# Performance work log

Measured on AMD Instinct MI355X. Metric: run time of the kernel, lower is better.

## Reference

```python
import jax, jax.numpy as jnp
import numpy as np

N, E, B_GRAPHS = 50000, 512000, 64
XD, ED, C, H, L = 16, 8, 64, 2, 2
EPS = 1e-5


def setup_inputs() -> dict:
    key = jax.random.key(0)
    ks = jax.random.split(key, 20)
    w = lambda k, shape: jax.random.normal(k, shape, jnp.float32) * 0.1
    return {
        "x": jax.random.normal(ks[0], (N, XD), jnp.float32),
        "edge_attr": jax.random.normal(ks[1], (E, ED), jnp.float32),
        "edge_src": jax.random.randint(ks[2], (E,), 0, N, dtype=jnp.int32),
        "edge_dst": jax.random.randint(ks[3], (E,), 0, N, dtype=jnp.int32),
        "batch": jnp.sort(jax.random.randint(ks[4], (N,), 0, B_GRAPHS, dtype=jnp.int32)),
        "node_W": w(ks[5], (XD, C)), "node_b": jnp.zeros((C,), jnp.float32),
        "edge_W": w(ks[6], (ED, C)), "edge_b": jnp.zeros((C,), jnp.float32),
        "Wq": w(ks[7], (L, C, H * C)), "bq": jnp.zeros((L, H * C), jnp.float32),
        "Wk": w(ks[8], (L, C, H * C)), "bk": jnp.zeros((L, H * C), jnp.float32),
        "Wv": w(ks[9], (L, C, H * C)), "bv": jnp.zeros((L, H * C), jnp.float32),
        "We": w(ks[10], (L, C, H * C)), "be": jnp.zeros((L, H * C), jnp.float32),
        "Wskip": w(ks[11], (L, C, C)), "bskip": jnp.zeros((L, C), jnp.float32),
        "gamma": jnp.ones((L, C), jnp.float32), "beta": jnp.zeros((L, C), jnp.float32),
        "gate_W": w(ks[12], (C, 1)), "gate_b": jnp.zeros((1,), jnp.float32),
        "out_W": w(ks[13], (C, 1)), "out_b": jnp.zeros((1,), jnp.float32),
    }


def reference(x, edge_attr, edge_src, edge_dst, batch,
              node_W, node_b, edge_W, edge_b,
              Wq, bq, Wk, bk, Wv, bv, We, be,
              Wskip, bskip, gamma, beta,
              gate_W, gate_b, out_W, out_b):
    n = x.shape[0]
    h = x @ node_W + node_b                       # node encoder: [N, C]
    e = edge_attr @ edge_W + edge_b               # edge encoder: [E, C]
    scale = 1.0 / jnp.sqrt(jnp.float32(C))
    for i in range(L):
        identity = h
        # TransformerConv (UniMP), concat=False -> mean over heads
        q = (h @ Wq[i] + bq[i]).reshape(n, H, C)
        k = (h @ Wk[i] + bk[i]).reshape(n, H, C)
        v = (h @ Wv[i] + bv[i]).reshape(n, H, C)
        ep = (e @ We[i] + be[i]).reshape(-1, H, C)
        k_e = k[edge_src] + ep                    # [E, H, C]
        v_e = v[edge_src] + ep                    # [E, H, C]
        logits = jnp.einsum('ehc,ehc->eh', q[edge_dst], k_e) * scale
        # segment softmax over incoming edges of each target node
        m = jax.ops.segment_max(logits, edge_dst, num_segments=n)
        a = jnp.exp(logits - m[edge_dst])
        denom = jax.ops.segment_sum(a, edge_dst, num_segments=n)
        alpha = a / denom[edge_dst]               # [E, H]
        agg = jax.ops.segment_sum(alpha[:, :, None] * v_e, edge_dst, num_segments=n)
        out = agg.mean(axis=1) + h @ Wskip[i] + bskip[i]   # root/skip term
        # BatchNorm1d (training mode, biased variance)
        mu = out.mean(axis=0)
        var = out.var(axis=0)
        out = gamma[i] * (out - mu) * jax.lax.rsqrt(var + EPS) + beta[i]
        out = jax.nn.leaky_relu(out, 0.01)
        h = out + identity                        # residual
    # GlobalAttention pooling over graphs
    gate = (h @ gate_W + gate_b)[:, 0]            # [N]
    gm = jax.ops.segment_max(gate, batch, num_segments=B_GRAPHS)
    ge = jnp.exp(gate - gm[batch])
    gd = jax.ops.segment_sum(ge, batch, num_segments=B_GRAPHS)
    wts = ge / gd[batch]
    pooled = jax.ops.segment_sum(wts[:, None] * h, batch, num_segments=B_GRAPHS)
    return jax.nn.sigmoid(pooled @ out_W + out_b)  # [B_GRAPHS, 1]
```

## Files before the change

### kernel.cpp

```cpp
#include <hip/hip_runtime.h>
#include <hip/hip_bf16.h>

typedef unsigned short ushort_t;
typedef __attribute__((ext_vector_type(8))) short short8;
typedef __attribute__((ext_vector_type(4))) float float4v;

__device__ __forceinline__ float bfu_lo(unsigned u) {
    return __uint_as_float(u << 16);
}
__device__ __forceinline__ float bfu_hi(unsigned u) {
    return __uint_as_float(u & 0xffff0000u);
}
__device__ __forceinline__ ushort_t f2bf(float f) {
    __hip_bfloat16 h = __float2bfloat16(f);
    return *reinterpret_cast<ushort_t*>(&h);
}



__global__ __launch_bounds__(256) void setup_kernel(
    const float* __restrict__ x, const float* __restrict__ node_W,
    const float* __restrict__ node_b,
    const float* __restrict__ edge_W, const float* __restrict__ edge_b,
    const float* __restrict__ We, const float* __restrict__ be,
    const float* __restrict__ Wq, const float* __restrict__ bq,
    const float* __restrict__ Wk, const float* __restrict__ bk,
    const float* __restrict__ Wv, const float* __restrict__ bv,
    const float* __restrict__ Wskip, const float* __restrict__ bskip,
    float* __restrict__ h, ushort_t* __restrict__ h_bf,
    int* __restrict__ counts,
    float* __restrict__ Wc, float* __restrict__ bcb,
    ushort_t* __restrict__ Wall_arr, float* __restrict__ Wall_bias,
    int O0, int O1, int O2, int N) {
    int b = blockIdx.x, t = threadIdx.x;
    if (b < O0) {
        int idx = b * 256 + t;
        if (idx < N * 64) {
            int n = idx >> 6, c = idx & 63;
            float acc = node_b[c];
#pragma unroll
            for (int j = 0; j < 16; ++j) acc += x[n * 16 + j] * node_W[j * 64 + c];
            h[idx] = acc;
            h_bf[idx] = f2bf(acc);
        }
    } else if (b < O1) {
        int i = (b - O0) * 256 + t;
        if (i < N) counts[i] = 0;
    } else if (b < O2) {
        int tid = (b - O1) * 256 + t;
        if (tid < 2048) {
            int l = tid >> 10, d = (tid >> 7) & 7, j = tid & 127;
            float s = 0.f;
            for (int m = 0; m < 64; ++m) s += edge_W[d * 64 + m] * We[l * 8192 + m * 128 + j];
            Wc[l * 1024 + d * 128 + j] = s;
        } else if (tid < 2048 + 256) {
            int u = tid - 2048;
            int l = u >> 7, j = u & 127;
            float s = be[l * 128 + j];
            for (int m = 0; m < 64; ++m) s += edge_b[m] * We[l * 8192 + m * 128 + j];
            bcb[l * 128 + j] = s;
        }
    } else {
        int tid = (b - O2) * 256 + t;
        if (tid < 2 * 28672) {
            int l = tid / 28672, u = tid % 28672;
            int j = u & 7, ln = (u >> 3) & 63, kch = (u >> 9) & 1, ct = u >> 10;
            int nn = ln & 15, quad = ln >> 4;
            int k = kch * 32 + quad * 8 + j;
            int col = ct * 16 + nn;
            float v;
            if (col < 128)      v = Wq[l * 8192 + k * 128 + col];
            else if (col < 256) v = Wk[l * 8192 + k * 128 + col - 128];
            else if (col < 384) v = Wv[l * 8192 + k * 128 + col - 256];
            else                v = Wskip[l * 4096 + k * 64 + col - 384];
            Wall_arr[(size_t)l * 32768 + ct * 1024 + kch * 512 + ln * 8 + j] = f2bf(v);
        } else if (tid < 2 * 28672 + 2 * 448) {
            int u = tid - 2 * 28672;
            int l = u / 448, col = u % 448;
            float v;
            if (col < 128)      v = bq[l * 128 + col];
            else if (col < 256) v = bk[l * 128 + col - 128];
            else if (col < 384) v = bv[l * 128 + col - 256];
            else                v = bskip[l * 64 + col - 384];
            Wall_bias[l * 512 + col] = v;
        }
    }
}

__global__ void combine2_kernel(const float* __restrict__ Wq, const float* __restrict__ bq,
                                const float* __restrict__ Wc, const float* __restrict__ bcb,
                                ushort_t* __restrict__ Wall_arr, float* __restrict__ Wall_bias) {
    int tid = blockIdx.x * 256 + threadIdx.x;
    if (tid < 2304) {
        int l = tid / 1152, u = tid % 1152, k = u / 18, j = u % 18;
        float s = 0.f;
        if (j < 16) {
            int hh = j >> 3, d = j & 7;
            for (int c = 0; c < 64; ++c)
                s += Wq[l * 8192 + k * 128 + hh * 64 + c] * Wc[l * 1024 + d * 128 + hh * 64 + c];
        } else {
            int hh = j - 16;
            for (int c = 0; c < 64; ++c)
                s += Wq[l * 8192 + k * 128 + hh * 64 + c] * bcb[l * 128 + hh * 64 + c];
        }
        s *= 0.125f;
        int col = 448 + j;
        int ct = col >> 4, nn = col & 15;
        int kch = k >> 5, quad = (k >> 3) & 3, jj = k & 7;
        int ln = quad * 16 + nn;
        Wall_arr[(size_t)l * 32768 + ct * 1024 + kch * 512 + ln * 8 + jj] = f2bf(s);
    } else if (tid < 2304 + 36) {
        int u = tid - 2304;
        int l = u / 18, j = u % 18;
        float s = 0.f;
        if (j < 16) {
            int hh = j >> 3, d = j & 7;
            for (int c = 0; c < 64; ++c)
                s += bq[l * 128 + hh * 64 + c] * Wc[l * 1024 + d * 128 + hh * 64 + c];
        } else {
            int hh = j - 16;
            for (int c = 0; c < 64; ++c)
                s += bq[l * 128 + hh * 64 + c] * bcb[l * 128 + hh * 64 + c];
        }
        Wall_bias[l * 512 + 448 + j] = 0.125f * s;
    }
}


__global__ void csr_count_kernel(const int* __restrict__ dst, int* __restrict__ counts, int E) {
    int e = blockIdx.x * 256 + threadIdx.x;
    if (e < E) atomicAdd(&counts[dst[e]], 1);
}

__global__ void scan1_kernel(const int* __restrict__ counts, int* __restrict__ rowptr,
                             int* __restrict__ bsums, int N) {
    __shared__ int s[256];
    int t = threadIdx.x, i = blockIdx.x * 256 + t;
    int v = (i < N) ? counts[i] : 0;
    s[t] = v;
    __syncthreads();
    for (int d = 1; d < 256; d <<= 1) {
        int x = (t >= d) ? s[t - d] : 0;
        __syncthreads();
        s[t] += x;
        __syncthreads();
    }
    if (i < N) rowptr[i] = s[t] - v;
    if (t == 255) bsums[blockIdx.x] = s[255];
}

__global__ void scan3_kernel(int* __restrict__ rowptr, const int* __restrict__ bsums,
                             int* __restrict__ cursor, int N, int E, int nb) {
    __shared__ int sh[256];
    int t = threadIdx.x;
    int v = (t < nb) ? bsums[t] : 0;
    sh[t] = v;
    __syncthreads();
    for (int d = 1; d < 256; d <<= 1) {
        int x = (t >= d) ? sh[t - d] : 0;
        __syncthreads();
        sh[t] += x;
        __syncthreads();
    }
    int blk = blockIdx.x;
    int offv = (blk == 0) ? 0 : sh[blk - 1];
    int i = blk * 256 + t;
    if (i < N) {
        int r = rowptr[i] + offv;
        rowptr[i] = r;
        cursor[i] = r;
    }
    if (i == 0) rowptr[N] = E;
}

__global__ void csr_fill_kernel(const int* __restrict__ dst, const int* __restrict__ src,
                                const float* __restrict__ edge_attr, int* __restrict__ cursor,
                                int* __restrict__ csr_src, float* __restrict__ ea_perm, int E) {
    int e = blockIdx.x * 256 + threadIdx.x;
    if (e < E) {
        int pos = atomicAdd(&cursor[dst[e]], 1);
        csr_src[pos] = src[e] * 768 + 256;
        float4 a0 = *(const float4*)(edge_attr + (size_t)e * 8);
        float4 a1 = *(const float4*)(edge_attr + (size_t)e * 8 + 4);
        *(float4*)(ea_perm + (size_t)pos * 8) = a0;
        *(float4*)(ea_perm + (size_t)pos * 8 + 4) = a1;
    }
}


__global__ __launch_bounds__(256) void qkv_mfma_kernel(
    const ushort_t* __restrict__ h_bf,
    const ushort_t* __restrict__ Wall_arr, const float* __restrict__ Wall_bias,
    ushort_t* __restrict__ qkv, float* __restrict__ outbuf, float* __restrict__ qcbuf, int N) {
    int wave = threadIdx.x >> 6, lane = threadIdx.x & 63;
    int quad = lane >> 4, nn = lane & 15;
    int n0 = blockIdx.x * 32;
    int nodeA = n0 + nn;       if (nodeA >= N) nodeA = N - 1;
    int nodeB = n0 + 16 + nn;  if (nodeB >= N) nodeB = N - 1;
    const ushort_t* apA = h_bf + (size_t)nodeA * 64 + quad * 8;
    const ushort_t* apB = h_bf + (size_t)nodeB * 64 + quad * 8;
    short8 aA0 = *(const short8*)apA;
    short8 aA1 = *(const short8*)(apA + 32);
    short8 aB0 = *(const short8*)apB;
    short8 aB1 = *(const short8*)(apB + 32);
    int ct_start = (wave < 2) ? wave * 8 : (16 + (wave - 2) * 7);
    int ct_cnt = (wave < 2) ? 8 : 7;
    for (int i = 0; i < ct_cnt; ++i) {
        int ct = ct_start + i;
        const ushort_t* bp = Wall_arr + (size_t)ct * 1024 + lane * 8;
        short8 b0 = *(const short8*)bp;
        short8 b1 = *(const short8*)(bp + 512);
        float4v cA = {0.f, 0.f, 0.f, 0.f};
        float4v cB = {0.f, 0.f, 0.f, 0.f};
        cA = __builtin_amdgcn_mfma_f32_16x16x32_bf16(aA0, b0, cA, 0, 0, 0);
        cA = __builtin_amdgcn_mfma_f32_16x16x32_bf16(aA1, b1, cA, 0, 0, 0);
        cB = __builtin_amdgcn_mfma_f32_16x16x32_bf16(aB0, b0, cB, 0, 0, 0);
        cB = __builtin_amdgcn_mfma_f32_16x16x32_bf16(aB1, b1, cB, 0, 0, 0);
        int col = ct * 16 + nn;
        float bias = Wall_bias[col];
#pragma unroll
        for (int g = 0; g < 2; ++g) {
            float4v c = (g == 0) ? cA : cB;
            int nbase = n0 + g * 16 + quad * 4;
            if (col < 384) {
                int cm;
                if (col < 128) cm = col;
                else if (col < 256) { int cc = col - 128; cm = 128 + ((cc >> 1) << 2) + (cc & 1); }
                else { int cc = col - 256; cm = 128 + ((cc >> 1) << 2) + 2 + (cc & 1); }
                ushort_t* qp = qkv + (size_t)nbase * 384 + cm;
#pragma unroll
                for (int r = 0; r < 4; ++r)
                    if (nbase + r < N) qp[(size_t)r * 384] = f2bf(c[r] + bias);
            } else if (col < 448) {
                float* op = outbuf + (size_t)nbase * 64 + (col - 448 + 64);
#pragma unroll
                for (int r = 0; r < 4; ++r)
                    if (nbase + r < N) op[(size_t)r * 64] = c[r] + bias;
            } else if (col < 466) {
                float* qp2 = qcbuf + (size_t)nbase * 20 + (col - 448);
#pragma unroll
                for (int r = 0; r < 4; ++r)
                    if (nbase + r < N) qp2[(size_t)r * 20] = c[r] + bias;
            }
        }
    }
}


__global__ __launch_bounds__(256) void bnqkv_kernel(
    const float* __restrict__ outbuf_in, const float* __restrict__ bnsums,
    const float* __restrict__ gamma, const float* __restrict__ beta,
    float* __restrict__ h,
    const ushort_t* __restrict__ Wall_arr, const float* __restrict__ Wall_bias,
    ushort_t* __restrict__ qkv, float* __restrict__ outbuf, float* __restrict__ qcbuf, int N) {
    __shared__ ushort_t hb[32 * 64];
    __shared__ float ss_scale[64], ss_shift[64];
    int t = threadIdx.x;
    if (t < 64) {
        float invN = 1.f / (float)N;
        float mean = bnsums[t] * invN;
        float var = bnsums[64 + t] * invN - mean * mean;
        float sc = gamma[t] * rsqrtf(var + 1e-5f);
        ss_scale[t] = sc;
        ss_shift[t] = beta[t] - mean * sc;
    }
    __syncthreads();
    int n0 = blockIdx.x * 32;
    int c = t & 63;
    float sc = ss_scale[c], sh = ss_shift[c];
#pragma unroll
    for (int i = 0; i < 8; ++i) {
        int li = t + i * 256;
        int gidx = n0 * 64 + li;
        float hn = 0.f;
        if (gidx < N * 64) {
            float o = outbuf_in[gidx] * sc + sh;
            o = (o > 0.f) ? o : 0.01f * o;
            hn = h[gidx] + o;
            h[gidx] = hn;
        }
        hb[li] = f2bf(hn);
    }
    __syncthreads();
    int wave = t >> 6, lane = t & 63;
    int quad = lane >> 4, nn = lane & 15;
    const ushort_t* apA = hb + nn * 64 + quad * 8;
    const ushort_t* apB = hb + (16 + nn) * 64 + quad * 8;
    short8 aA0 = *(const short8*)apA;
    short8 aA1 = *(const short8*)(apA + 32);
    short8 aB0 = *(const short8*)apB;
    short8 aB1 = *(const short8*)(apB + 32);
    int ct_start = (wave < 2) ? wave * 8 : (16 + (wave - 2) * 7);
    int ct_cnt = (wave < 2) ? 8 : 7;
    for (int i = 0; i < ct_cnt; ++i) {
        int ct = ct_start + i;
        const ushort_t* bp = Wall_arr + (size_t)ct * 1024 + lane * 8;
        short8 b0 = *(const short8*)bp;
        short8 b1 = *(const short8*)(bp + 512);
        float4v cA = {0.f, 0.f, 0.f, 0.f};
        float4v cB = {0.f, 0.f, 0.f, 0.f};
        cA = __builtin_amdgcn_mfma_f32_16x16x32_bf16(aA0, b0, cA, 0, 0, 0);
        cA = __builtin_amdgcn_mfma_f32_16x16x32_bf16(aA1, b1, cA, 0, 0, 0);
        cB = __builtin_amdgcn_mfma_f32_16x16x32_bf16(aB0, b0, cB, 0, 0, 0);
        cB = __builtin_amdgcn_mfma_f32_16x16x32_bf16(aB1, b1, cB, 0, 0, 0);
        int col = ct * 16 + nn;
        float bias = Wall_bias[col];
#pragma unroll
        for (int g = 0; g < 2; ++g) {
            float4v cc2 = (g == 0) ? cA : cB;
            int nbase = n0 + g * 16 + quad * 4;
            if (col < 384) {
                int cm;
                if (col < 128) cm = col;
                else if (col < 256) { int cv = col - 128; cm = 128 + ((cv >> 1) << 2) + (cv & 1); }
                else { int cv = col - 256; cm = 128 + ((cv >> 1) << 2) + 2 + (cv & 1); }
                ushort_t* qp = qkv + (size_t)nbase * 384 + cm;
#pragma unroll
                for (int r = 0; r < 4; ++r)
                    if (nbase + r < N) qp[(size_t)r * 384] = f2bf(cc2[r] + bias);
            } else if (col < 448) {
                float* op = outbuf + (size_t)nbase * 64 + (col - 448 + 64);
#pragma unroll
                for (int r = 0; r < 4; ++r)
                    if (nbase + r < N) op[(size_t)r * 64] = cc2[r] + bias;
            } else if (col < 466) {
                float* qp2 = qcbuf + (size_t)nbase * 20 + (col - 448);
#pragma unroll
                for (int r = 0; r < 4; ++r)
                    if (nbase + r < N) qp2[(size_t)r * 20] = cc2[r] + bias;
            }
        }
    }
}


__global__ __launch_bounds__(256) void attn_kernel(
    const ushort_t* __restrict__ qkv, const float* __restrict__ qcbuf,
    const int* __restrict__ csr_src, const float* __restrict__ ea_perm,
    const int* __restrict__ rowptr,
    const float* __restrict__ Wc, const float* __restrict__ bcb,
    float* __restrict__ outbuf, float* __restrict__ part, int N) {
    __shared__ float Wc_s[1024];
    __shared__ float bc_s[128];
    __shared__ float stat[4][4][2][64];
    int t = threadIdx.x;
    for (int i = t; i < 1024; i += 256) Wc_s[i] = Wc[i];
    if (t < 128) bc_s[t] = bcb[t];
    {
        float* sf = &stat[0][0][0][0];
        for (int i = t; i < 2048; i += 256) sf[i] = 0.f;
    }
    __syncthreads();
    int lane = t & 63, wid = t >> 6;
    int grp = lane >> 4, l16 = lane & 15;
    int head = l16 >> 3, l8 = l16 & 7;
    const char* qkvb = (const char*)qkv;

    int n = blockIdx.x * 16 + wid * 4 + grp;
    bool active = (n < N);
    int nn = active ? n : (N - 1);
    int start = rowptr[nn];
    int end = rowptr[nn + 1];
    int deg = active ? (end - start) : 0;
    int wdeg = deg;
    wdeg = max(wdeg, __shfl_xor(wdeg, 16));
    wdeg = max(wdeg, __shfl_xor(wdeg, 32));

    float lsum = 0.f;
    float vacc[8] = {0.f, 0.f, 0.f, 0.f, 0.f, 0.f, 0.f, 0.f};
    float se[8]   = {0.f, 0.f, 0.f, 0.f, 0.f, 0.f, 0.f, 0.f};

    if (wdeg > 0) {
        uint4 qr = *(const uint4*)(qkvb + (size_t)nn * 768 + 16 * l16);
        float qf0 = bfu_lo(qr.x), qf1 = bfu_hi(qr.x);
        float qf2 = bfu_lo(qr.y), qf3 = bfu_hi(qr.y);
        float qf4 = bfu_lo(qr.z), qf5 = bfu_hi(qr.z);
        float qf6 = bfu_lo(qr.w), qf7 = bfu_hi(qr.w);
        const float* qcp = qcbuf + (size_t)nn * 20;
        float4 qcA = *(const float4*)(qcp + head * 8);
        float4 qcB = *(const float4*)(qcp + head * 8 + 4);
        float qb = qcp[16 + head];

        int offL = csr_src[(deg > 0) ? (start + min(l16, deg - 1)) : 0];
        int o0 = __shfl(offL, grp * 16);
        uint4 ca = *(const uint4*)(qkvb + (size_t)(unsigned)o0 + 32 * l16);
        uint4 cb = *(const uint4*)(qkvb + (size_t)(unsigned)o0 + 32 * l16 + 16);
        int gi0 = (deg > 0) ? start : 0;
        float4 e0 = *(const float4*)(ea_perm + (size_t)gi0 * 8);
        float4 e1 = *(const float4*)(ea_perm + (size_t)gi0 * 8 + 4);

        for (int it = 0; it < wdeg; ++it) {
            int itn = it + 1;
            if ((itn & 15) == 0) {
                offL = csr_src[(deg > 0) ? (start + min(itn + l16, deg - 1)) : 0];
            }
            int itc = min(itn, wdeg - 1);
            int on = __shfl(offL, grp * 16 + (itc & 15));
            uint4 na = *(const uint4*)(qkvb + (size_t)(unsigned)on + 32 * l16);
            uint4 nb2 = *(const uint4*)(qkvb + (size_t)(unsigned)on + 32 * l16 + 16);
            int gin = (deg > 0) ? (start + min(itc, deg - 1)) : 0;
            float4 f0 = *(const float4*)(ea_perm + (size_t)gin * 8);
            float4 f1 = *(const float4*)(ea_perm + (size_t)gin * 8 + 4);

            float dt = qf0 * bfu_lo(ca.x) + qf1 * bfu_hi(ca.x)
                     + qf2 * bfu_lo(ca.z) + qf3 * bfu_hi(ca.z)
                     + qf4 * bfu_lo(cb.x) + qf5 * bfu_hi(cb.x)
                     + qf6 * bfu_lo(cb.z) + qf7 * bfu_hi(cb.z);
            dt += __shfl_xor(dt, 1);
            dt += __shfl_xor(dt, 2);
            dt += __shfl_xor(dt, 4);
            float s0 = dt * 0.125f
                     + qcA.x * e0.x + qcA.y * e0.y + qcA.z * e0.z + qcA.w * e0.w
                     + qcB.x * e1.x + qcB.y * e1.y + qcB.z * e1.z + qcB.w * e1.w
                     + qb;
            float p = (it < deg) ? __expf(fmaxf(s0, -60.f)) : 0.f;
            lsum += p;
            vacc[0] += p * bfu_lo(ca.y); vacc[1] += p * bfu_hi(ca.y);
            vacc[2] += p * bfu_lo(ca.w); vacc[3] += p * bfu_hi(ca.w);
            vacc[4] += p * bfu_lo(cb.y); vacc[5] += p * bfu_hi(cb.y);
            vacc[6] += p * bfu_lo(cb.w); vacc[7] += p * bfu_hi(cb.w);
            se[0] += p * e0.x; se[1] += p * e0.y; se[2] += p * e0.z; se[3] += p * e0.w;
            se[4] += p * e1.x; se[5] += p * e1.y; se[6] += p * e1.z; se[7] += p * e1.w;
            ca = na; cb = nb2; e0 = f0; e1 = f1;
        }
    }

    if (active) {
        float inv = (deg > 0) ? (1.f / lsum) : 0.f;
        int jb = head * 64 + 8 * l8;
        float outv[8];
#pragma unroll
        for (int k2 = 0; k2 < 8; ++k2) {
            int j = jb + k2;
            float wv = lsum * bc_s[j];
#pragma unroll
            for (int m = 0; m < 8; ++m) wv += se[m] * Wc_s[m * 128 + j];
            float ox = (vacc[k2] + wv) * inv;
            float po = __shfl_xor(ox, 8);
            outv[k2] = 0.5f * (ox + po);
        }
        if (head == 0) {
            float* op = outbuf + (size_t)nn * 64 + 8 * l8;
            float4 c0 = *(const float4*)op;
            float4 c1 = *(const float4*)(op + 4);
            float fr[8];
            fr[0] = c0.x + outv[0]; fr[1] = c0.y + outv[1];
            fr[2] = c0.z + outv[2]; fr[3] = c0.w + outv[3];
            fr[4] = c1.x + outv[4]; fr[5] = c1.y + outv[5];
            fr[6] = c1.z + outv[6]; fr[7] = c1.w + outv[7];
            if (deg > 0) {
                *(float4*)op = make_float4(fr[0], fr[1], fr[2], fr[3]);
                *(float4*)(op + 4) = make_float4(fr[4], fr[5], fr[6], fr[7]);
            }
            float* sa = &stat[wid][grp][0][8 * l8];
            float* sq = &stat[wid][grp][1][8 * l8];
#pragma unroll
            for (int k2 = 0; k2 < 8; ++k2) {
                sa[k2] += fr[k2];
                sq[k2] += fr[k2] * fr[k2];
            }
        }
    }
    __syncthreads();
    if (t < 128) {
        int c = t & 63, qq = t >> 6;
        float s = 0.f;
#pragma unroll
        for (int w2 = 0; w2 < 4; ++w2)
#pragma unroll
            for (int g2 = 0; g2 < 4; ++g2) s += stat[w2][g2][qq][c];
        part[(size_t)blockIdx.x * 128 + t] = s;
    }
}


__global__ __launch_bounds__(256) void bnreduce_kernel(const float* __restrict__ part,
                                                       float* __restrict__ bnsums, int nb) {
    int s = blockIdx.x;
    int t = threadIdx.x;
    float a = 0.f;
    for (int b = t; b < nb; b += 256) a += part[(size_t)b * 128 + s];
    __shared__ float sh[256];
    sh[t] = a;
    __syncthreads();
    for (int d = 128; d; d >>= 1) {
        if (t < d) sh[t] += sh[t + d];
        __syncthreads();
    }
    if (t == 0) bnsums[s] = sh[0];
}

__global__ __launch_bounds__(256) void bnapply_kernel(
    const float* __restrict__ outbuf, const float* __restrict__ bnsums,
    const float* __restrict__ gamma, const float* __restrict__ beta,
    const float* __restrict__ gate_W, const float* __restrict__ gate_b,
    float* __restrict__ h, float* __restrict__ gatebuf, int N) {
    int idx = blockIdx.x * 256 + threadIdx.x;
    if (idx >= N * 64) return;
    int c = idx & 63, n = idx >> 6;
    float invN = 1.f / (float)N;
    float mean = bnsums[c] * invN;
    float var = bnsums[64 + c] * invN - mean * mean;
    float scale = gamma[c] * rsqrtf(var + 1e-5f);
    float shift = beta[c] - mean * scale;
    float o = outbuf[idx] * scale + shift;
    o = (o > 0.f) ? o : 0.01f * o;
    float hn = h[idx] + o;
    h[idx] = hn;
    float g = hn * gate_W[c];
#pragma unroll
    for (int off = 32; off; off >>= 1) g += __shfl_xor(g, off);
    if (c == 0) gatebuf[n] = g + gate_b[0];
}


__global__ __launch_bounds__(256) void pool_acc_kernel(
    const float* __restrict__ h, const float* __restrict__ gatebuf,
    const int* __restrict__ batch,
    float* __restrict__ pacc, float* __restrict__ pden, int N) {
    int b = blockIdx.x >> 3, chunk = blockIdx.x & 7;
    int lo = 0, hi = N;
    while (lo < hi) { int mid = (lo + hi) >> 1; if (batch[mid] < b) lo = mid + 1; else hi = mid; }
    int start = lo;
    lo = start; hi = N;
    while (lo < hi) { int mid = (lo + hi) >> 1; if (batch[mid] <= b) lo = mid + 1; else hi = mid; }
    int end = lo;
    int t = threadIdx.x, lane = t & 63, wid = t >> 6;
    __shared__ float sm[4];
    float mx = -1e30f;
    for (int n = start + t; n < end; n += 256) mx = fmaxf(mx, gatebuf[n]);
#pragma unroll
    for (int off = 32; off; off >>= 1) mx = fmaxf(mx, __shfl_xor(mx, off));
    if (lane == 0) sm[wid] = mx;
    __syncthreads();
    float mb = fmaxf(fmaxf(sm[0], sm[1]), fmaxf(sm[2], sm[3]));
    int gwid = chunk * 4 + wid;
    float acc = 0.f, den = 0.f;
    for (int n = start + gwid; n < end; n += 32) {
        float ge = __expf(gatebuf[n] - mb);
        acc += ge * h[(size_t)n * 64 + lane];
        den += ge;
    }
    __shared__ float sacc[4][64];
    __shared__ float sden[4];
    sacc[wid][lane] = acc;
    if (lane == 0) sden[wid] = den;
    __syncthreads();
    if (wid == 0) {
        pacc[(size_t)blockIdx.x * 64 + lane] =
            sacc[0][lane] + sacc[1][lane] + sacc[2][lane] + sacc[3][lane];
        if (lane == 0) pden[blockIdx.x] = sden[0] + sden[1] + sden[2] + sden[3];
    }
}

__global__ void pool_fin_kernel(const float* __restrict__ pacc, const float* __restrict__ pden,
                                const float* __restrict__ out_W, const float* __restrict__ out_b,
                                float* __restrict__ out) {
    int b = blockIdx.x, c = threadIdx.x;
    float pc = 0.f, dv = 0.f;
#pragma unroll
    for (int j = 0; j < 8; ++j) {
        pc += pacc[(size_t)(b * 8 + j) * 64 + c];
        dv += pden[b * 8 + j];
    }
    float s = pc * out_W[c];
#pragma unroll
    for (int off = 32; off; off >>= 1) s += __shfl_xor(s, off);
    if (c == 0) {
        if (dv <= 0.f) dv = 1.f;
        float v = s / dv + out_b[0];
        out[b] = 1.f / (1.f + __expf(-v));
    }
}


extern "C" void kernel_launch(void* const* d_in, const int* in_sizes, int n_in,
                              void* d_out, int out_size, void* d_ws, size_t ws_size,
                              hipStream_t stream) {
    const float* x         = (const float*)d_in[0];
    const float* edge_attr = (const float*)d_in[1];
    const int*   edge_src  = (const int*)d_in[2];
    const int*   edge_dst  = (const int*)d_in[3];
    const int*   batch     = (const int*)d_in[4];
    const float* node_W    = (const float*)d_in[5];
    const float* node_b    = (const float*)d_in[6];
    const float* edge_W    = (const float*)d_in[7];
    const float* edge_b    = (const float*)d_in[8];
    const float* Wq        = (const float*)d_in[9];
    const float* bq        = (const float*)d_in[10];
    const float* Wk        = (const float*)d_in[11];
    const float* bk        = (const float*)d_in[12];
    const float* Wv        = (const float*)d_in[13];
    const float* bv        = (const float*)d_in[14];
    const float* We        = (const float*)d_in[15];
    const float* be        = (const float*)d_in[16];
    const float* Wskip     = (const float*)d_in[17];
    const float* bskip     = (const float*)d_in[18];
    const float* gamma     = (const float*)d_in[19];
    const float* beta      = (const float*)d_in[20];
    const float* gate_W    = (const float*)d_in[21];
    const float* gate_b    = (const float*)d_in[22];
    const float* out_W     = (const float*)d_in[23];
    const float* out_b     = (const float*)d_in[24];
    float* out = (float*)d_out;

    const int N = in_sizes[0] / 16;
    const int E = in_sizes[2];
    const int nba = (N + 15) / 16;

    char* ws = (char*)d_ws;
    size_t off = 0;
    auto alloc = [&](size_t bytes) {
        size_t o = off;
        off += (bytes + 255) & ~(size_t)255;
        return o;
    };
    float*    h        = (float*)(ws + alloc((size_t)N * 64 * 4));
    ushort_t* h_bf     = (ushort_t*)(ws + alloc((size_t)N * 64 * 2));
    ushort_t* qkv      = (ushort_t*)(ws + alloc((size_t)N * 384 * 2));
    float*    outbuf   = (float*)(ws + alloc((size_t)N * 64 * 4));
    float*    qcbuf    = (float*)(ws + alloc((size_t)N * 20 * 4));
    int*      rowptr   = (int*)(ws + alloc((size_t)(N + 1) * 4));
    int*      cursor   = (int*)(ws + alloc((size_t)N * 4));
    int*      counts   = (int*)(ws + alloc((size_t)N * 4));
    int*      bsums    = (int*)(ws + alloc(1024));
    int*      csr_src  = (int*)(ws + alloc((size_t)E * 4));
    float*    ea_perm  = (float*)(ws + alloc((size_t)E * 8 * 4));
    float*    Wc       = (float*)(ws + alloc(2 * 1024 * 4));
    float*    bcb      = (float*)(ws + alloc(2 * 128 * 4));
    ushort_t* Wall_arr = (ushort_t*)(ws + alloc(2 * 32768 * 2));
    float*    Wall_b   = (float*)(ws + alloc(2 * 512 * 4));
    float*    bnsums   = (float*)(ws + alloc(128 * 4));
    float*    gatebuf  = (float*)(ws + alloc((size_t)N * 4));
    float*    pacc     = (float*)(ws + alloc((size_t)nba * 128 * 4));
    float*    pden     = (float*)(ws + alloc(512 * 4));
    if (off > ws_size) return;

    int O0 = (N * 64 + 255) / 256;
    int O1 = O0 + (N + 255) / 256;
    int O2 = O1 + 9;
    int O3 = O2 + 228;
    setup_kernel<<<O3, 256, 0, stream>>>(
        x, node_W, node_b, edge_W, edge_b, We, be, Wq, bq, Wk, bk, Wv, bv, Wskip, bskip,
        h, h_bf, counts, Wc, bcb, Wall_arr, Wall_b, O0, O1, O2, N);
    combine2_kernel<<<10, 256, 0, stream>>>(Wq, bq, Wc, bcb, Wall_arr, Wall_b);

    csr_count_kernel<<<(E + 255) / 256, 256, 0, stream>>>(edge_dst, counts, E);
    int nb = (N + 255) / 256;
    scan1_kernel<<<nb, 256, 0, stream>>>(counts, rowptr, bsums, N);
    scan3_kernel<<<nb, 256, 0, stream>>>(rowptr, bsums, cursor, N, E, nb);
    csr_fill_kernel<<<(E + 255) / 256, 256, 0, stream>>>(edge_dst, edge_src, edge_attr,
                                                         cursor, csr_src, ea_perm, E);

    qkv_mfma_kernel<<<(N + 31) / 32, 256, 0, stream>>>(
        h_bf, Wall_arr, Wall_b, qkv, outbuf, qcbuf, N);
    attn_kernel<<<nba, 256, 0, stream>>>(qkv, qcbuf, csr_src, ea_perm,
                                         rowptr, Wc, bcb, outbuf, pacc, N);
    bnreduce_kernel<<<128, 256, 0, stream>>>(pacc, bnsums, nba);
    bnqkv_kernel<<<(N + 31) / 32, 256, 0, stream>>>(
        outbuf, bnsums, gamma, beta, h,
        Wall_arr + 32768, Wall_b + 512, qkv, outbuf, qcbuf, N);

    attn_kernel<<<nba, 256, 0, stream>>>(qkv, qcbuf, csr_src, ea_perm,
                                         rowptr, Wc + 1024, bcb + 128,
                                         outbuf, pacc, N);
    bnreduce_kernel<<<128, 256, 0, stream>>>(pacc, bnsums, nba);
    bnapply_kernel<<<(N * 64 + 255) / 256, 256, 0, stream>>>(
        outbuf, bnsums, gamma + 64, beta + 64, gate_W, gate_b, h, gatebuf, N);

    pool_acc_kernel<<<512, 256, 0, stream>>>(h, gatebuf, batch, pacc, pden, N);
    pool_fin_kernel<<<64, 64, 0, stream>>>(pacc, pden, out_W, out_b, out);
}
```

Baseline: 383.2 us.

## Gather raw bf16 node features in attention and apply K/V projections algebraically

Per-edge K and V projections are replaced with the raw 64-wide bf16 node features of the source. Wq·Wk^T is folded into a per-node query vector (qk2), so logits become a dot product with gathered h. Softmax-weighted sums of h and of edge attributes are accumulated per node, then a new MFMA kernel (vapply) applies Wv and the edge projection afterwards, adding constant bias terms. This shrinks the per-edge gather from 768 to 128 bytes and cuts the node GEMM width, at the cost of an extra kernel launch and intermediate buffers.

```diff
diff --git a/kernel.cpp b/kernel.cpp
--- a/kernel.cpp
+++ b/kernel.cpp
@@ -31,6 +31,7 @@
     int* __restrict__ counts,
     float* __restrict__ Wc, float* __restrict__ bcb,
     ushort_t* __restrict__ Wall_arr, float* __restrict__ Wall_bias,
+    ushort_t* __restrict__ wv_arr,
     int O0, int O1, int O2, int N) {
     int b = blockIdx.x, t = threadIdx.x;
     if (b < O0) {
@@ -62,34 +63,57 @@
         }
     } else {
         int tid = (b - O2) * 256 + t;
-        if (tid < 2 * 28672) {
-            int l = tid / 28672, u = tid % 28672;
+        if (tid < 2 * 14336) {
+            int l = tid / 14336, u = tid % 14336;
             int j = u & 7, ln = (u >> 3) & 63, kch = (u >> 9) & 1, ct = u >> 10;
             int nn = ln & 15, quad = ln >> 4;
             int k = kch * 32 + quad * 8 + j;
             int col = ct * 16 + nn;
-            float v;
-            if (col < 128)      v = Wq[l * 8192 + k * 128 + col];
-            else if (col < 256) v = Wk[l * 8192 + k * 128 + col - 128];
-            else if (col < 384) v = Wv[l * 8192 + k * 128 + col - 256];
-            else                v = Wskip[l * 4096 + k * 64 + col - 384];
-            Wall_arr[(size_t)l * 32768 + ct * 1024 + kch * 512 + ln * 8 + j] = f2bf(v);
-        } else if (tid < 2 * 28672 + 2 * 448) {
-            int u = tid - 2 * 28672;
-            int l = u / 448, col = u % 448;
-            float v;
-            if (col < 128)      v = bq[l * 128 + col];
-            else if (col < 256) v = bk[l * 128 + col - 128];
-            else if (col < 384) v = bv[l * 128 + col - 256];
-            else                v = bskip[l * 64 + col - 384];
-            Wall_bias[l * 512 + col] = v;
+            float v = 0.f;
+            if (col < 128) {
+                int hh = col >> 6, m = col & 63;
+                const float* wq = Wq + l * 8192 + k * 128 + hh * 64;
+                const float* wk = Wk + l * 8192 + m * 128 + hh * 64;
+                float s = 0.f;
+                for (int c2 = 0; c2 < 64; ++c2) s += wq[c2] * wk[c2];
+                v = 0.125f * s;
+            } else if (col < 192) {
+                v = Wskip[l * 4096 + k * 64 + (col - 128)];
+            }
+            Wall_arr[(size_t)l * 14336 + ct * 1024 + kch * 512 + ln * 8 + j] = f2bf(v);
+        } else if (tid < 2 * 14336 + 2 * 224) {
+            int u = tid - 2 * 14336;
+            int l = u / 224, col = u % 224;
+            float v = 0.f;
+            if (col < 128) {
+                int hh = col >> 6, m = col & 63;
+                const float* bqp = bq + l * 128 + hh * 64;
+                const float* wk = Wk + l * 8192 + m * 128 + hh * 64;
+                float s = 0.f;
+                for (int c2 = 0; c2 < 64; ++c2) s += bqp[c2] * wk[c2];
+                v = 0.125f * s;
+            } else if (col < 192) {
+                v = bskip[l * 64 + col - 128];
+            }
+            Wall_bias[l * 224 + col] = v;
+        } else if (tid < 2 * 14336 + 2 * 224 + 2 * 8192) {
+            int u = tid - (2 * 14336 + 2 * 224);
+            int l = u >> 13, r = u & 8191;
+            int j = r & 7, ln = (r >> 3) & 63, ct = (r >> 9) & 3, kc = r >> 11;
+            int quad = ln >> 4, nn = ln & 15;
+            int p = kc * 32 + quad * 8 + j;
+            int hh = p >> 6, m = p & 63;
+            int c2 = ct * 16 + nn;
+            wv_arr[(size_t)l * 8192 + r] = f2bf(Wv[l * 8192 + m * 128 + hh * 64 + c2]);
         }
     }
 }
 
 __global__ void combine2_kernel(const float* __restrict__ Wq, const float* __restrict__ bq,
+                                const float* __restrict__ bk, const float* __restrict__ bv,
                                 const float* __restrict__ Wc, const float* __restrict__ bcb,
-                                ushort_t* __restrict__ Wall_arr, float* __restrict__ Wall_bias) {
+                                ushort_t* __restrict__ Wall_arr, float* __restrict__ Wall_bias,
+                                float* __restrict__ cst) {
     int tid = blockIdx.x * 256 + threadIdx.x;
     if (tid < 2304) {
         int l = tid / 1152, u = tid % 1152, k = u / 18, j = u % 18;
@@ -101,14 +125,15 @@
         } else {
             int hh = j - 16;
             for (int c = 0; c < 64; ++c)
-                s += Wq[l * 8192 + k * 128 + hh * 64 + c] * bcb[l * 128 + hh * 64 + c];
+                s += Wq[l * 8192 + k * 128 + hh * 64 + c] *
+                     (bcb[l * 128 + hh * 64 + c] + bk[l * 128 + hh * 64 + c]);
         }
         s *= 0.125f;
-        int col = 448 + j;
+        int col = 192 + j;
         int ct = col >> 4, nn = col & 15;
         int kch = k >> 5, quad = (k >> 3) & 3, jj = k & 7;
         int ln = quad * 16 + nn;
-        Wall_arr[(size_t)l * 32768 + ct * 1024 + kch * 512 + ln * 8 + jj] = f2bf(s);
+        Wall_arr[(size_t)l * 14336 + ct * 1024 + kch * 512 + ln * 8 + jj] = f2bf(s);
     } else if (tid < 2304 + 36) {
         int u = tid - 2304;
         int l = u / 18, j = u % 18;
@@ -120,9 +145,15 @@
         } else {
             int hh = j - 16;
             for (int c = 0; c < 64; ++c)
-                s += bq[l * 128 + hh * 64 + c] * bcb[l * 128 + hh * 64 + c];
-        }
-        Wall_bias[l * 512 + 448 + j] = 0.125f * s;
+                s += bq[l * 128 + hh * 64 + c] *
+                     (bcb[l * 128 + hh * 64 + c] + bk[l * 128 + hh * 64 + c]);
+        }
+        Wall_bias[l * 224 + 192 + j] = 0.125f * s;
+    } else if (tid < 2304 + 36 + 128) {
+        int u = tid - 2340;
+        int l = u >> 6, c = u & 63;
+        cst[l * 64 + c] = 0.5f * (bv[l * 128 + c] + bv[l * 128 + 64 + c] +
+                                  bcb[l * 128 + c] + bcb[l * 128 + 64 + c]);
     }
 }
 
@@ -179,7 +210,7 @@
     int e = blockIdx.x * 256 + threadIdx.x;
     if (e < E) {
         int pos = atomicAdd(&cursor[dst[e]], 1);
-        csr_src[pos] = src[e] * 768 + 256;
+        csr_src[pos] = src[e] * 128;
         float4 a0 = *(const float4*)(edge_attr + (size_t)e * 8);
         float4 a1 = *(const float4*)(edge_attr + (size_t)e * 8 + 4);
         *(float4*)(ea_perm + (size_t)pos * 8) = a0;
@@ -188,10 +219,32 @@
 }
 
 
+__device__ __forceinline__ void gemm_store(
+    int col, float bias, float4v c, int nbase, int N,
+    ushort_t* __restrict__ qk2buf, float* __restrict__ outbuf, float* __restrict__ qcbuf) {
+    if (col < 128) {
+        ushort_t* qp = qk2buf + (size_t)nbase * 128 + col;
+#pragma unroll
+        for (int r = 0; r < 4; ++r)
+            if (nbase + r < N) qp[(size_t)r * 128] = f2bf(c[r] + bias);
+    } else if (col < 192) {
+        float* op = outbuf + (size_t)nbase * 64 + (col - 128);
+#pragma unroll
+        for (int r = 0; r < 4; ++r)
+            if (nbase + r < N) op[(size_t)r * 64] = c[r] + bias;
+    } else if (col < 210) {
+        float* qp2 = qcbuf + (size_t)nbase * 20 + (col - 192);
+#pragma unroll
+        for (int r = 0; r < 4; ++r)
+            if (nbase + r < N) qp2[(size_t)r * 20] = c[r] + bias;
+    }
+}
+
 __global__ __launch_bounds__(256) void qkv_mfma_kernel(
     const ushort_t* __restrict__ h_bf,
     const ushort_t* __restrict__ Wall_arr, const float* __restrict__ Wall_bias,
-    ushort_t* __restrict__ qkv, float* __restrict__ outbuf, float* __restrict__ qcbuf, int N) {
+    ushort_t* __restrict__ qk2buf, float* __restrict__ outbuf, float* __restrict__ qcbuf,
+    int N) {
     int wave = threadIdx.x >> 6, lane = threadIdx.x & 63;
     int quad = lane >> 4, nn = lane & 15;
     int n0 = blockIdx.x * 32;
@@ -203,8 +256,8 @@
     short8 aA1 = *(const short8*)(apA + 32);
     short8 aB0 = *(const short8*)apB;
     short8 aB1 = *(const short8*)(apB + 32);
-    int ct_start = (wave < 2) ? wave * 8 : (16 + (wave - 2) * 7);
-    int ct_cnt = (wave < 2) ? 8 : 7;
+    int ct_start = (wave < 2) ? wave * 4 : (8 + (wave - 2) * 3);
+    int ct_cnt = (wave < 2) ? 4 : 3;
     for (int i = 0; i < ct_cnt; ++i) {
         int ct = ct_start + i;
         const ushort_t* bp = Wall_arr + (size_t)ct * 1024 + lane * 8;
@@ -218,31 +271,8 @@
         cB = __builtin_amdgcn_mfma_f32_16x16x32_bf16(aB1, b1, cB, 0, 0, 0);
         int col = ct * 16 + nn;
         float bias = Wall_bias[col];
-#pragma unroll
-        for (int g = 0; g < 2; ++g) {
-            float4v c = (g == 0) ? cA : cB;
-            int nbase = n0 + g * 16 + quad * 4;
-            if (col < 384) {
-                int cm;
-                if (col < 128) cm = col;
-                else if (col < 256) { int cc = col - 128; cm = 128 + ((cc >> 1) << 2) + (cc & 1); }
-                else { int cc = col - 256; cm = 128 + ((cc >> 1) << 2) + 2 + (cc & 1); }
-                ushort_t* qp = qkv + (size_t)nbase * 384 + cm;
-#pragma unroll
-                for (int r = 0; r < 4; ++r)
-                    if (nbase + r < N) qp[(size_t)r * 384] = f2bf(c[r] + bias);
-            } else if (col < 448) {
-                float* op = outbuf + (size_t)nbase * 64 + (col - 448 + 64);
-#pragma unroll
-                for (int r = 0; r < 4; ++r)
-                    if (nbase + r < N) op[(size_t)r * 64] = c[r] + bias;
-            } else if (col < 466) {
-                float* qp2 = qcbuf + (size_t)nbase * 20 + (col - 448);
-#pragma unroll
-                for (int r = 0; r < 4; ++r)
-                    if (nbase + r < N) qp2[(size_t)r * 20] = c[r] + bias;
-            }
-        }
+        gemm_store(col, bias, cA, n0 + quad * 4, N, qk2buf, outbuf, qcbuf);
+        gemm_store(col, bias, cB, n0 + 16 + quad * 4, N, qk2buf, outbuf, qcbuf);
     }
 }
 
@@ -250,9 +280,10 @@
 __global__ __launch_bounds__(256) void bnqkv_kernel(
     const float* __restrict__ outbuf_in, const float* __restrict__ bnsums,
     const float* __restrict__ gamma, const float* __restrict__ beta,
-    float* __restrict__ h,
+    float* __restrict__ h, ushort_t* __restrict__ h_bf,
     const ushort_t* __restrict__ Wall_arr, const float* __restrict__ Wall_bias,
-    ushort_t* __restrict__ qkv, float* __restrict__ outbuf, float* __restrict__ qcbuf, int N) {
+    ushort_t* __restrict__ qk2buf, float* __restrict__ outbuf, float* __restrict__ qcbuf,
+    int N) {
     __shared__ ushort_t hb[32 * 64];
     __shared__ float ss_scale[64], ss_shift[64];
     int t = threadIdx.x;
@@ -278,6 +309,7 @@
             o = (o > 0.f) ? o : 0.01f * o;
             hn = h[gidx] + o;
             h[gidx] = hn;
+            h_bf[gidx] = f2bf(hn);
         }
         hb[li] = f2bf(hn);
     }
@@ -290,8 +322,8 @@
     short8 aA1 = *(const short8*)(apA + 32);
     short8 aB0 = *(const short8*)apB;
     short8 aB1 = *(const short8*)(apB + 32);
-    int ct_start = (wave < 2) ? wave * 8 : (16 + (wave - 2) * 7);
-    int ct_cnt = (wave < 2) ? 8 : 7;
+    int ct_start = (wave < 2) ? wave * 4 : (8 + (wave - 2) * 3);
+    int ct_cnt = (wave < 2) ? 4 : 3;
     for (int i = 0; i < ct_cnt; ++i) {
         int ct = ct_start + i;
         const ushort_t* bp = Wall_arr + (size_t)ct * 1024 + lane * 8;
@@ -305,172 +337,185 @@
         cB = __builtin_amdgcn_mfma_f32_16x16x32_bf16(aB1, b1, cB, 0, 0, 0);
         int col = ct * 16 + nn;
         float bias = Wall_bias[col];
-#pragma unroll
-        for (int g = 0; g < 2; ++g) {
-            float4v cc2 = (g == 0) ? cA : cB;
-            int nbase = n0 + g * 16 + quad * 4;
-            if (col < 384) {
-                int cm;
-                if (col < 128) cm = col;
-                else if (col < 256) { int cv = col - 128; cm = 128 + ((cv >> 1) << 2) + (cv & 1); }
-                else { int cv = col - 256; cm = 128 + ((cv >> 1) << 2) + 2 + (cv & 1); }
-                ushort_t* qp = qkv + (size_t)nbase * 384 + cm;
-#pragma unroll
-                for (int r = 0; r < 4; ++r)
-                    if (nbase + r < N) qp[(size_t)r * 384] = f2bf(cc2[r] + bias);
-            } else if (col < 448) {
-                float* op = outbuf + (size_t)nbase * 64 + (col - 448 + 64);
-#pragma unroll
-                for (int r = 0; r < 4; ++r)
-                    if (nbase + r < N) op[(size_t)r * 64] = cc2[r] + bias;
-            } else if (col < 466) {
-                float* qp2 = qcbuf + (size_t)nbase * 20 + (col - 448);
-#pragma unroll
-                for (int r = 0; r < 4; ++r)
-                    if (nbase + r < N) qp2[(size_t)r * 20] = cc2[r] + bias;
-            }
-        }
+        gemm_store(col, bias, cA, n0 + quad * 4, N, qk2buf, outbuf, qcbuf);
+        gemm_store(col, bias, cB, n0 + 16 + quad * 4, N, qk2buf, outbuf, qcbuf);
     }
 }
 
 
 __global__ __launch_bounds__(256) void attn_kernel(
-    const ushort_t* __restrict__ qkv, const float* __restrict__ qcbuf,
+    const ushort_t* __restrict__ h_bf, const ushort_t* __restrict__ qk2buf,
+    const float* __restrict__ qcbuf,
     const int* __restrict__ csr_src, const float* __restrict__ ea_perm,
     const int* __restrict__ rowptr,
-    const float* __restrict__ Wc, const float* __restrict__ bcb,
-    float* __restrict__ outbuf, float* __restrict__ part, int N) {
-    __shared__ float Wc_s[1024];
-    __shared__ float bc_s[128];
-    __shared__ float stat[4][4][2][64];
+    ushort_t* __restrict__ haccn, float* __restrict__ sen, float* __restrict__ degw,
+    int N) {
     int t = threadIdx.x;
-    for (int i = t; i < 1024; i += 256) Wc_s[i] = Wc[i];
-    if (t < 128) bc_s[t] = bcb[t];
-    {
-        float* sf = &stat[0][0][0][0];
-        for (int i = t; i < 2048; i += 256) sf[i] = 0.f;
-    }
-    __syncthreads();
     int lane = t & 63, wid = t >> 6;
     int grp = lane >> 4, l16 = lane & 15;
     int head = l16 >> 3, l8 = l16 & 7;
-    const char* qkvb = (const char*)qkv;
+    const char* hbb = (const char*)h_bf;
 
     int n = blockIdx.x * 16 + wid * 4 + grp;
     bool active = (n < N);
     int nn = active ? n : (N - 1);
     int start = rowptr[nn];
-    int end = rowptr[nn + 1];
-    int deg = active ? (end - start) : 0;
+    int deg = active ? (rowptr[nn + 1] - start) : 0;
     int wdeg = deg;
     wdeg = max(wdeg, __shfl_xor(wdeg, 16));
     wdeg = max(wdeg, __shfl_xor(wdeg, 32));
 
     float lsum = 0.f;
-    float vacc[8] = {0.f, 0.f, 0.f, 0.f, 0.f, 0.f, 0.f, 0.f};
+    float hacc[8] = {0.f, 0.f, 0.f, 0.f, 0.f, 0.f, 0.f, 0.f};
     float se[8]   = {0.f, 0.f, 0.f, 0.f, 0.f, 0.f, 0.f, 0.f};
 
     if (wdeg > 0) {
-        uint4 qr = *(const uint4*)(qkvb + (size_t)nn * 768 + 16 * l16);
-        float qf0 = bfu_lo(qr.x), qf1 = bfu_hi(qr.x);
-        float qf2 = bfu_lo(qr.y), qf3 = bfu_hi(qr.y);
-        float qf4 = bfu_lo(qr.z), qf5 = bfu_hi(qr.z);
-        float qf6 = bfu_lo(qr.w), qf7 = bfu_hi(qr.w);
+        uint4 qr = *(const uint4*)((const char*)qk2buf + (size_t)nn * 256 + head * 128 + l8 * 16);
+        float qk0 = bfu_lo(qr.x), qk1 = bfu_hi(qr.x);
+        float qk2f = bfu_lo(qr.y), qk3 = bfu_hi(qr.y);
+        float qk4 = bfu_lo(qr.z), qk5 = bfu_hi(qr.z);
+        float qk6 = bfu_lo(qr.w), qk7 = bfu_hi(qr.w);
         const float* qcp = qcbuf + (size_t)nn * 20;
         float4 qcA = *(const float4*)(qcp + head * 8);
         float4 qcB = *(const float4*)(qcp + head * 8 + 4);
         float qb = qcp[16 + head];
 
-        int offL = csr_src[(deg > 0) ? (start + min(l16, deg - 1)) : 0];
+        bool dpos = (deg > 0);
+        int dclamp = dpos ? (deg - 1) : 0;
+
+        int offL = csr_src[dpos ? (start + min(l16, dclamp)) : 0];
         int o0 = __shfl(offL, grp * 16);
-        uint4 ca = *(const uint4*)(qkvb + (size_t)(unsigned)o0 + 32 * l16);
-        uint4 cb = *(const uint4*)(qkvb + (size_t)(unsigned)o0 + 32 * l16 + 16);
-        int gi0 = (deg > 0) ? start : 0;
+        uint4 ca = *(const uint4*)(hbb + (size_t)(unsigned)o0 + l8 * 16);
+        int gi0 = dpos ? start : 0;
         float4 e0 = *(const float4*)(ea_perm + (size_t)gi0 * 8);
         float4 e1 = *(const float4*)(ea_perm + (size_t)gi0 * 8 + 4);
 
         for (int it = 0; it < wdeg; ++it) {
             int itn = it + 1;
-            if ((itn & 15) == 0) {
-                offL = csr_src[(deg > 0) ? (start + min(itn + l16, deg - 1)) : 0];
-            }
+            if ((itn & 15) == 0)
+                offL = csr_src[dpos ? (start + min(itn + l16, dclamp)) : 0];
             int itc = min(itn, wdeg - 1);
             int on = __shfl(offL, grp * 16 + (itc & 15));
-            uint4 na = *(const uint4*)(qkvb + (size_t)(unsigned)on + 32 * l16);
-            uint4 nb2 = *(const uint4*)(qkvb + (size_t)(unsigned)on + 32 * l16 + 16);
-            int gin = (deg > 0) ? (start + min(itc, deg - 1)) : 0;
+            uint4 na = *(const uint4*)(hbb + (size_t)(unsigned)on + l8 * 16);
+            int gin = dpos ? (start + min(itc, dclamp)) : 0;
             float4 f0 = *(const float4*)(ea_perm + (size_t)gin * 8);
             float4 f1 = *(const float4*)(ea_perm + (size_t)gin * 8 + 4);
 
-            float dt = qf0 * bfu_lo(ca.x) + qf1 * bfu_hi(ca.x)
-                     + qf2 * bfu_lo(ca.z) + qf3 * bfu_hi(ca.z)
-                     + qf4 * bfu_lo(cb.x) + qf5 * bfu_hi(cb.x)
-                     + qf6 * bfu_lo(cb.z) + qf7 * bfu_hi(cb.z);
+            float h0 = bfu_lo(ca.x), h1 = bfu_hi(ca.x);
+            float h2 = bfu_lo(ca.y), h3 = bfu_hi(ca.y);
+            float h4 = bfu_lo(ca.z), h5 = bfu_hi(ca.z);
+            float h6 = bfu_lo(ca.w), h7 = bfu_hi(ca.w);
+            float dt = qk0 * h0 + qk1 * h1 + qk2f * h2 + qk3 * h3
+                     + qk4 * h4 + qk5 * h5 + qk6 * h6 + qk7 * h7;
             dt += __shfl_xor(dt, 1);
             dt += __shfl_xor(dt, 2);
             dt += __shfl_xor(dt, 4);
-            float s0 = dt * 0.125f
+            float s0 = dt
                      + qcA.x * e0.x + qcA.y * e0.y + qcA.z * e0.z + qcA.w * e0.w
                      + qcB.x * e1.x + qcB.y * e1.y + qcB.z * e1.z + qcB.w * e1.w
                      + qb;
             float p = (it < deg) ? __expf(fmaxf(s0, -60.f)) : 0.f;
             lsum += p;
-            vacc[0] += p * bfu_lo(ca.y); vacc[1] += p * bfu_hi(ca.y);
-            vacc[2] += p * bfu_lo(ca.w); vacc[3] += p * bfu_hi(ca.w);
-            vacc[4] += p * bfu_lo(cb.y); vacc[5] += p * bfu_hi(cb.y);
-            vacc[6] += p * bfu_lo(cb.w); vacc[7] += p * bfu_hi(cb.w);
+            hacc[0] += p * h0; hacc[1] += p * h1;
+            hacc[2] += p * h2; hacc[3] += p * h3;
+            hacc[4] += p * h4; hacc[5] += p * h5;
+            hacc[6] += p * h6; hacc[7] += p * h7;
             se[0] += p * e0.x; se[1] += p * e0.y; se[2] += p * e0.z; se[3] += p * e0.w;
             se[4] += p * e1.x; se[5] += p * e1.y; se[6] += p * e1.z; se[7] += p * e1.w;
-            ca = na; cb = nb2; e0 = f0; e1 = f1;
+            ca = na; e0 = f0; e1 = f1;
         }
     }
 
     if (active) {
-        float inv = (deg > 0) ? (1.f / lsum) : 0.f;
-        int jb = head * 64 + 8 * l8;
-        float outv[8];
-#pragma unroll
-        for (int k2 = 0; k2 < 8; ++k2) {
-            int j = jb + k2;
-            float wv = lsum * bc_s[j];
-#pragma unroll
-            for (int m = 0; m < 8; ++m) wv += se[m] * Wc_s[m * 128 + j];
-            float ox = (vacc[k2] + wv) * inv;
-            float po = __shfl_xor(ox, 8);
-            outv[k2] = 0.5f * (ox + po);
-        }
-        if (head == 0) {
-            float* op = outbuf + (size_t)nn * 64 + 8 * l8;
-            float4 c0 = *(const float4*)op;
-            float4 c1 = *(const float4*)(op + 4);
-            float fr[8];
-            fr[0] = c0.x + outv[0]; fr[1] = c0.y + outv[1];
-            fr[2] = c0.z + outv[2]; fr[3] = c0.w + outv[3];
-            fr[4] = c1.x + outv[4]; fr[5] = c1.y + outv[5];
-            fr[6] = c1.z + outv[6]; fr[7] = c1.w + outv[7];
-            if (deg > 0) {
-                *(float4*)op = make_float4(fr[0], fr[1], fr[2], fr[3]);
-                *(float4*)(op + 4) = make_float4(fr[4], fr[5], fr[6], fr[7]);
+        float inv = (deg > 0) ? (0.5f / lsum) : 0.f;
+        unsigned pw0 = (unsigned)f2bf(hacc[0] * inv) | ((unsigned)f2bf(hacc[1] * inv) << 16);
+        unsigned pw1 = (unsigned)f2bf(hacc[2] * inv) | ((unsigned)f2bf(hacc[3] * inv) << 16);
+        unsigned pw2 = (unsigned)f2bf(hacc[4] * inv) | ((unsigned)f2bf(hacc[5] * inv) << 16);
+        unsigned pw3 = (unsigned)f2bf(hacc[6] * inv) | ((unsigned)f2bf(hacc[7] * inv) << 16);
+        uint4 pk = make_uint4(pw0, pw1, pw2, pw3);
+        *(uint4*)((char*)haccn + (size_t)nn * 256 + head * 128 + l8 * 16) = pk;
+        if (l8 == 0) {
+            *(float4*)(sen + (size_t)nn * 16 + head * 8) =
+                make_float4(se[0] * inv, se[1] * inv, se[2] * inv, se[3] * inv);
+            *(float4*)(sen + (size_t)nn * 16 + head * 8 + 4) =
+                make_float4(se[4] * inv, se[5] * inv, se[6] * inv, se[7] * inv);
+            if (head == 0) degw[nn] = (deg > 0) ? 1.f : 0.f;
+        }
+    }
+}
+
+
+__global__ __launch_bounds__(256) void vapply_kernel(
+    const ushort_t* __restrict__ haccn, const float* __restrict__ sen,
+    const float* __restrict__ degw,
+    const ushort_t* __restrict__ wv_arr, const float* __restrict__ Wc,
+    const float* __restrict__ cst,
+    float* __restrict__ outbuf, float* __restrict__ part, int N) {
+    __shared__ float Wc_s[1024];
+    __shared__ float cst_s[64];
+    __shared__ float sen_s[32][16];
+    __shared__ float dw_s[32];
+    __shared__ float ps[128];
+    int t = threadIdx.x;
+    for (int i = t; i < 1024; i += 256) Wc_s[i] = Wc[i];
+    if (t < 64) cst_s[t] = cst[t];
+    int n0 = blockIdx.x * 32;
+    for (int i = t; i < 512; i += 256) {
+        int ln2 = i >> 4;
+        int nc = n0 + ln2; if (nc >= N) nc = N - 1;
+        sen_s[ln2][i & 15] = sen[(size_t)nc * 16 + (i & 15)];
+    }
+    if (t < 32) {
+        int nc = n0 + t; if (nc >= N) nc = N - 1;
+        dw_s[t] = degw[nc];
+    }
+    __syncthreads();
+    int wave = t >> 6, lane = t & 63;
+    int quad = lane >> 4, nn = lane & 15;
+    int nodeA = n0 + nn;       if (nodeA >= N) nodeA = N - 1;
+    int nodeB = n0 + 16 + nn;  if (nodeB >= N) nodeB = N - 1;
+    int ct = wave;
+    float4v cA = {0.f, 0.f, 0.f, 0.f};
+    float4v cB = {0.f, 0.f, 0.f, 0.f};
+#pragma unroll
+    for (int kc = 0; kc < 4; ++kc) {
+        short8 aA = *(const short8*)(haccn + (size_t)nodeA * 128 + kc * 32 + quad * 8);
+        short8 aB = *(const short8*)(haccn + (size_t)nodeB * 128 + kc * 32 + quad * 8);
+        short8 bb = *(const short8*)(wv_arr + kc * 2048 + ct * 512 + lane * 8);
+        cA = __builtin_amdgcn_mfma_f32_16x16x32_bf16(aA, bb, cA, 0, 0, 0);
+        cB = __builtin_amdgcn_mfma_f32_16x16x32_bf16(aB, bb, cB, 0, 0, 0);
+    }
+    int col = ct * 16 + nn;
+    float sa = 0.f, sq = 0.f;
+#pragma unroll
+    for (int g = 0; g < 2; ++g) {
+        float4v acc = g ? cB : cA;
+        int lbase = g * 16 + quad * 4;
+#pragma unroll
+        for (int r = 0; r < 4; ++r) {
+            int ln2 = lbase + r;
+            int nr = n0 + ln2;
+            const float* sp = sen_s[ln2];
+            float ep = 0.f;
+#pragma unroll
+            for (int hh = 0; hh < 2; ++hh)
+#pragma unroll
+                for (int d = 0; d < 8; ++d)
+                    ep += sp[hh * 8 + d] * Wc_s[d * 128 + hh * 64 + col];
+            if (nr < N) {
+                float val = acc[r] + ep + dw_s[ln2] * cst_s[col] +
+                            outbuf[(size_t)nr * 64 + col];
+                outbuf[(size_t)nr * 64 + col] = val;
+                sa += val;
+                sq += val * val;
             }
-            float* sa = &stat[wid][grp][0][8 * l8];
-            float* sq = &stat[wid][grp][1][8 * l8];
-#pragma unroll
-            for (int k2 = 0; k2 < 8; ++k2) {
-                sa[k2] += fr[k2];
-                sq[k2] += fr[k2] * fr[k2];
-            }
-        }
-    }
-    __syncthreads();
-    if (t < 128) {
-        int c = t & 63, qq = t >> 6;
-        float s = 0.f;
-#pragma unroll
-        for (int w2 = 0; w2 < 4; ++w2)
-#pragma unroll
-            for (int g2 = 0; g2 < 4; ++g2) s += stat[w2][g2][qq][c];
-        part[(size_t)blockIdx.x * 128 + t] = s;
-    }
+        }
+    }
+    sa += __shfl_xor(sa, 16); sa += __shfl_xor(sa, 32);
+    sq += __shfl_xor(sq, 16); sq += __shfl_xor(sq, 32);
+    if (quad == 0) { ps[col] = sa; ps[64 + col] = sq; }
+    __syncthreads();
+    if (t < 128) part[(size_t)blockIdx.x * 128 + t] = ps[t];
 }
 
 
@@ -607,6 +652,7 @@
     const int N = in_sizes[0] / 16;
     const int E = in_sizes[2];
     const int nba = (N + 15) / 16;
+    const int nbv = (N + 31) / 32;
 
     char* ws = (char*)d_ws;
     size_t off = 0;
@@ -617,9 +663,12 @@
     };
     float*    h        = (float*)(ws + alloc((size_t)N * 64 * 4));
     ushort_t* h_bf     = (ushort_t*)(ws + alloc((size_t)N * 64 * 2));
-    ushort_t* qkv      = (ushort_t*)(ws + alloc((size_t)N * 384 * 2));
+    ushort_t* qk2buf   = (ushort_t*)(ws + alloc((size_t)N * 128 * 2));
     float*    outbuf   = (float*)(ws + alloc((size_t)N * 64 * 4));
     float*    qcbuf    = (float*)(ws + alloc((size_t)N * 20 * 4));
+    ushort_t* haccn    = (ushort_t*)(ws + alloc((size_t)N * 128 * 2));
+    float*    sen      = (float*)(ws + alloc((size_t)N * 16 * 4));
+    float*    degw     = (float*)(ws + alloc((size_t)N * 4));
     int*      rowptr   = (int*)(ws + alloc((size_t)(N + 1) * 4));
     int*      cursor   = (int*)(ws + alloc((size_t)N * 4));
     int*      counts   = (int*)(ws + alloc((size_t)N * 4));
@@ -628,22 +677,25 @@
     float*    ea_perm  = (float*)(ws + alloc((size_t)E * 8 * 4));
     float*    Wc       = (float*)(ws + alloc(2 * 1024 * 4));
     float*    bcb      = (float*)(ws + alloc(2 * 128 * 4));
-    ushort_t* Wall_arr = (ushort_t*)(ws + alloc(2 * 32768 * 2));
-    float*    Wall_b   = (float*)(ws + alloc(2 * 512 * 4));
+    ushort_t* Wall_arr = (ushort_t*)(ws + alloc(2 * 14336 * 2));
+    float*    Wall_b   = (float*)(ws + alloc(2 * 224 * 4));
+    ushort_t* wv_arr   = (ushort_t*)(ws + alloc(2 * 8192 * 2));
+    float*    cst      = (float*)(ws + alloc(2 * 64 * 4));
     float*    bnsums   = (float*)(ws + alloc(128 * 4));
     float*    gatebuf  = (float*)(ws + alloc((size_t)N * 4));
-    float*    pacc     = (float*)(ws + alloc((size_t)nba * 128 * 4));
+    float*    part     = (float*)(ws + alloc((size_t)nbv * 128 * 4));
+    float*    pacc     = (float*)(ws + alloc((size_t)512 * 64 * 4));
     float*    pden     = (float*)(ws + alloc(512 * 4));
     if (off > ws_size) return;
 
     int O0 = (N * 64 + 255) / 256;
     int O1 = O0 + (N + 255) / 256;
     int O2 = O1 + 9;
-    int O3 = O2 + 228;
+    int O3 = O2 + 178;
     setup_kernel<<<O3, 256, 0, stream>>>(
         x, node_W, node_b, edge_W, edge_b, We, be, Wq, bq, Wk, bk, Wv, bv, Wskip, bskip,
-        h, h_bf, counts, Wc, bcb, Wall_arr, Wall_b, O0, O1, O2, N);
-    combine2_kernel<<<10, 256, 0, stream>>>(Wq, bq, Wc, bcb, Wall_arr, Wall_b);
+        h, h_bf, counts, Wc, bcb, Wall_arr, Wall_b, wv_arr, O0, O1, O2, N);
+    combine2_kernel<<<10, 256, 0, stream>>>(Wq, bq, bk, bv, Wc, bcb, Wall_arr, Wall_b, cst);
 
     csr_count_kernel<<<(E + 255) / 256, 256, 0, stream>>>(edge_dst, counts, E);
     int nb = (N + 255) / 256;
@@ -652,19 +704,22 @@
     csr_fill_kernel<<<(E + 255) / 256, 256, 0, stream>>>(edge_dst, edge_src, edge_attr,
                                                          cursor, csr_src, ea_perm, E);
 
-    qkv_mfma_kernel<<<(N + 31) / 32, 256, 0, stream>>>(
-        h_bf, Wall_arr, Wall_b, qkv, outbuf, qcbuf, N);
-    attn_kernel<<<nba, 256, 0, stream>>>(qkv, qcbuf, csr_src, ea_perm,
-                                         rowptr, Wc, bcb, outbuf, pacc, N);
-    bnreduce_kernel<<<128, 256, 0, stream>>>(pacc, bnsums, nba);
-    bnqkv_kernel<<<(N + 31) / 32, 256, 0, stream>>>(
-        outbuf, bnsums, gamma, beta, h,
-        Wall_arr + 32768, Wall_b + 512, qkv, outbuf, qcbuf, N);
-
-    attn_kernel<<<nba, 256, 0, stream>>>(qkv, qcbuf, csr_src, ea_perm,
-                                         rowptr, Wc + 1024, bcb + 128,
-                                         outbuf, pacc, N);
-    bnreduce_kernel<<<128, 256, 0, stream>>>(pacc, bnsums, nba);
+    qkv_mfma_kernel<<<nbv, 256, 0, stream>>>(
+        h_bf, Wall_arr, Wall_b, qk2buf, outbuf, qcbuf, N);
+    attn_kernel<<<nba, 256, 0, stream>>>(h_bf, qk2buf, qcbuf, csr_src, ea_perm,
+                                         rowptr, haccn, sen, degw, N);
+    vapply_kernel<<<nbv, 256, 0, stream>>>(haccn, sen, degw, wv_arr, Wc, cst,
+                                           outbuf, part, N);
+    bnreduce_kernel<<<128, 256, 0, stream>>>(part, bnsums, nbv);
+    bnqkv_kernel<<<nbv, 256, 0, stream>>>(
+        outbuf, bnsums, gamma, beta, h, h_bf,
+        Wall_arr + 14336, Wall_b + 224, qk2buf, outbuf, qcbuf, N);
+
+    attn_kernel<<<nba, 256, 0, stream>>>(h_bf, qk2buf, qcbuf, csr_src, ea_perm,
+                                         rowptr, haccn, sen, degw, N);
+    vapply_kernel<<<nbv, 256, 0, stream>>>(haccn, sen, degw, wv_arr + 8192, Wc + 1024,
+                                           cst + 64, outbuf, part, N);
+    bnreduce_kernel<<<128, 256, 0, stream>>>(part, bnsums, nbv);
     bnapply_kernel<<<(N * 64 + 255) / 256, 256, 0, stream>>>(
         outbuf, bnsums, gamma + 64, beta + 64, gate_W, gate_b, h, gatebuf, N);
 
```

Result: faster. 352.9 us (-7.9%).
